# Performance work log

Measured on AMD Instinct MI355X. Metric: run time of the kernel, lower is better.

Reference implementation:

```python
import jax, jax.numpy as jnp
import numpy as np
from jax import lax

EPS = 1e-06
S = 0.025
ALPHA = 0.98
DELTA = 2.0
R = 0.5


def setup_inputs() -> dict:
    key = jax.random.key(0)
    # magnitude spectrogram: [batch, freq, time], nonnegative
    x = jax.random.uniform(key, (32, 256, 4096), dtype=jnp.float32)
    return {"x": x}


def reference(x):
    # x: [B, F, T]; EMA smoother runs over the time axis (last dim).
    # m_0 = s*x_0 ; m_t = (1-s)*m_{t-1} + s*x_t  (init carry 0 reproduces m_0 = s*x_0)
    xt = jnp.moveaxis(x, 2, 0)  # [T, B, F]

    def step(m, frame):
        m = (1.0 - S) * m + S * frame
        return m, m

    _, M = lax.scan(step, jnp.zeros_like(xt[0]), xt)  # [T, B, F]
    M = jnp.moveaxis(M, 0, 2)  # [B, F, T]
    # power-law compression fused elementwise
    return (x / (M + EPS) ** ALPHA + DELTA) ** R - DELTA ** R
```

## Files before the change

### kernel.cpp

```cpp
#include <hip/hip_runtime.h>


constexpr int T_LEN  = 4096;
constexpr int LANES  = 64;
constexpr int QUADS  = 4;
constexpr int PER_LANE = QUADS * 4;
constexpr int CHUNK  = LANES * PER_LANE;
constexpr int CHUNK_F4 = CHUNK / 4;
constexpr int NCHUNK = T_LEN / CHUNK;
constexpr int WAVES_PER_BLK = 4;
constexpr int NTHR   = LANES * WAVES_PER_BLK;

constexpr float EPSF = 1e-6f;
constexpr float SF   = 0.025f;
constexpr float A1F  = 0.975f;

constexpr double dA1    = 0.975;
constexpr double dA2    = dA1 * dA1;
constexpr double dA4    = dA2 * dA2;
constexpr double dA8    = dA4 * dA4;
constexpr double dA16   = dA8 * dA8;
constexpr double dA32   = dA16 * dA16;
constexpr double dA64   = dA32 * dA32;
constexpr double dA128  = dA64 * dA64;
constexpr double dA256  = dA128 * dA128;
constexpr double dA512  = dA256 * dA256;
constexpr double dA1024 = dA512 * dA512;

__global__ __launch_bounds__(NTHR, 6) void pcen_wave_kernel(
    const float* __restrict__ x, float* __restrict__ out, int rows)
{
    const int lane = threadIdx.x & 63;
    const int wave = threadIdx.x >> 6;
    const int row  = blockIdx.x * WAVES_PER_BLK + wave;
    if (row >= rows) return;

    const long long base = (long long)row * T_LEN;
    const float4* __restrict__ px   = (const float4*)(x + base);
    float4* __restrict__       pout = (float4*)(out + base);

    const float cA16  = (float)dA16;
    const float cA32  = (float)dA32;
    const float cA64  = (float)dA64;
    const float cA128 = (float)dA128;
    const float cA256 = (float)dA256;
    const float cA512 = (float)dA512;
    const float cA1024 = (float)dA1024;

    float flane = 1.0f;
    if (lane & 1)  flane *= cA16;
    if (lane & 2)  flane *= cA32;
    if (lane & 4)  flane *= cA64;
    if (lane & 8)  flane *= cA128;
    if (lane & 16) flane *= cA256;
    if (lane & 32) flane *= cA512;

    const float SQRT_D = 1.41421356237309515f;

    float4 buf[QUADS];
    {
        const float4* p = px + lane * QUADS;
#pragma unroll
        for (int j = 0; j < QUADS; ++j) buf[j] = p[j];
    }

    float carry = 0.0f;

#pragma unroll
    for (int c = 0; c < NCHUNK; ++c) {
        float4 nxt[QUADS];
        if (c < NCHUNK - 1) {
            const float4* p = px + (c + 1) * CHUNK_F4 + lane * QUADS;
#pragma unroll
            for (int j = 0; j < QUADS; ++j) nxt[j] = p[j];
        }

        float m = 0.0f;
#pragma unroll
        for (int j = 0; j < QUADS; ++j) {
            m = fmaf(A1F, m, SF * buf[j].x);
            m = fmaf(A1F, m, SF * buf[j].y);
            m = fmaf(A1F, m, SF * buf[j].z);
            m = fmaf(A1F, m, SF * buf[j].w);
        }
        float Sv = m;

        float t;
        t = __shfl_up(Sv, 1,  64); if (lane >= 1)  Sv = fmaf(cA16,  t, Sv);
        t = __shfl_up(Sv, 2,  64); if (lane >= 2)  Sv = fmaf(cA32,  t, Sv);
        t = __shfl_up(Sv, 4,  64); if (lane >= 4)  Sv = fmaf(cA64,  t, Sv);
        t = __shfl_up(Sv, 8,  64); if (lane >= 8)  Sv = fmaf(cA128, t, Sv);
        t = __shfl_up(Sv, 16, 64); if (lane >= 16) Sv = fmaf(cA256, t, Sv);
        t = __shfl_up(Sv, 32, 64); if (lane >= 32) Sv = fmaf(cA512, t, Sv);

        float excl = __shfl_up(Sv, 1, 64);
        if (lane == 0) excl = 0.0f;

        m = fmaf(flane, carry, excl);

        float last = __shfl(Sv, 63, 64);
        carry = fmaf(cA1024, carry, last);

        float4* q = pout + c * CHUNK_F4 + lane * QUADS;
#pragma unroll
        for (int j = 0; j < QUADS; ++j) {
            float4 v = buf[j];
            float4 o;
            m = fmaf(A1F, m, SF * v.x);
            o.x = __builtin_amdgcn_sqrtf(
                      fmaf(v.x, __builtin_amdgcn_exp2f(
                          -0.98f * __builtin_amdgcn_logf(m + EPSF)), 2.0f)) - SQRT_D;
            m = fmaf(A1F, m, SF * v.y);
            o.y = __builtin_amdgcn_sqrtf(
                      fmaf(v.y, __builtin_amdgcn_exp2f(
                          -0.98f * __builtin_amdgcn_logf(m + EPSF)), 2.0f)) - SQRT_D;
            m = fmaf(A1F, m, SF * v.z);
            o.z = __builtin_amdgcn_sqrtf(
                      fmaf(v.z, __builtin_amdgcn_exp2f(
                          -0.98f * __builtin_amdgcn_logf(m + EPSF)), 2.0f)) - SQRT_D;
            m = fmaf(A1F, m, SF * v.w);
            o.w = __builtin_amdgcn_sqrtf(
                      fmaf(v.w, __builtin_amdgcn_exp2f(
                          -0.98f * __builtin_amdgcn_logf(m + EPSF)), 2.0f)) - SQRT_D;
            q[j] = o;
        }

#pragma unroll
        for (int j = 0; j < QUADS; ++j) buf[j] = nxt[j];
    }
}

extern "C" void kernel_launch(void* const* d_in, const int* in_sizes, int n_in,
                              void* d_out, int out_size, void* d_ws, size_t ws_size,
                              hipStream_t stream) {
    const float* x = (const float*)d_in[0];
    float* out = (float*)d_out;
    const int rows = in_sizes[0] / T_LEN;
    const int blocks = (rows + WAVES_PER_BLK - 1) / WAVES_PER_BLK;
    pcen_wave_kernel<<<dim3(blocks), dim3(NTHR), 0, stream>>>(x, out, rows);
}
```

Measured before the change: 244.7 us.

## Use lane-contiguous float4 tiles with four independent wave scans per tile

Changes the per-lane data assignment so each lane owns one float4 per 256-element sub-tile, making each wave load and store fully contiguous 1 KB segments instead of each lane reading 64 contiguous bytes. It runs four independent shuffle scans per tile, which gives more ILP, and rescales the decay powers to match 4 elements per lane. It also raises the launch-bounds occupancy hint from 6 to 8. The cost is four times as many cross-lane shuffles per tile and a serial carry chain across the sub-tiles.

```diff
diff --git a/kernel.cpp b/kernel.cpp
--- a/kernel.cpp
+++ b/kernel.cpp
@@ -1,33 +1,30 @@
 #include <hip/hip_runtime.h>
 
 
-constexpr int T_LEN  = 4096;
-constexpr int LANES  = 64;
-constexpr int QUADS  = 4;
-constexpr int PER_LANE = QUADS * 4;
-constexpr int CHUNK  = LANES * PER_LANE;
-constexpr int CHUNK_F4 = CHUNK / 4;
-constexpr int NCHUNK = T_LEN / CHUNK;
+constexpr int T_LEN   = 4096;
+constexpr int LANES   = 64;
+constexpr int SUBS    = 4;
+constexpr int TILE    = LANES * 4 * SUBS;
+constexpr int TILE_F4 = TILE / 4;
+constexpr int NTILE   = T_LEN / TILE;
 constexpr int WAVES_PER_BLK = 4;
-constexpr int NTHR   = LANES * WAVES_PER_BLK;
+constexpr int NTHR    = LANES * WAVES_PER_BLK;
 
 constexpr float EPSF = 1e-6f;
 constexpr float SF   = 0.025f;
 constexpr float A1F  = 0.975f;
 
-constexpr double dA1    = 0.975;
-constexpr double dA2    = dA1 * dA1;
-constexpr double dA4    = dA2 * dA2;
-constexpr double dA8    = dA4 * dA4;
-constexpr double dA16   = dA8 * dA8;
-constexpr double dA32   = dA16 * dA16;
-constexpr double dA64   = dA32 * dA32;
-constexpr double dA128  = dA64 * dA64;
-constexpr double dA256  = dA128 * dA128;
-constexpr double dA512  = dA256 * dA256;
-constexpr double dA1024 = dA512 * dA512;
+constexpr double dA1   = 0.975;
+constexpr double dA2   = dA1 * dA1;
+constexpr double dA4   = dA2 * dA2;
+constexpr double dA8   = dA4 * dA4;
+constexpr double dA16  = dA8 * dA8;
+constexpr double dA32  = dA16 * dA16;
+constexpr double dA64  = dA32 * dA32;
+constexpr double dA128 = dA64 * dA64;
+constexpr double dA256 = dA128 * dA128;
 
-__global__ __launch_bounds__(NTHR, 6) void pcen_wave_kernel(
+__global__ __launch_bounds__(NTHR, 8) void pcen_wave_kernel(
     const float* __restrict__ x, float* __restrict__ out, int rows)
 {
     const int lane = threadIdx.x & 63;
@@ -39,72 +36,74 @@
     const float4* __restrict__ px   = (const float4*)(x + base);
     float4* __restrict__       pout = (float4*)(out + base);
 
+    const float cA4   = (float)dA4;
+    const float cA8   = (float)dA8;
     const float cA16  = (float)dA16;
     const float cA32  = (float)dA32;
     const float cA64  = (float)dA64;
     const float cA128 = (float)dA128;
     const float cA256 = (float)dA256;
-    const float cA512 = (float)dA512;
-    const float cA1024 = (float)dA1024;
 
     float flane = 1.0f;
-    if (lane & 1)  flane *= cA16;
-    if (lane & 2)  flane *= cA32;
-    if (lane & 4)  flane *= cA64;
-    if (lane & 8)  flane *= cA128;
-    if (lane & 16) flane *= cA256;
-    if (lane & 32) flane *= cA512;
+    if (lane & 1)  flane *= cA4;
+    if (lane & 2)  flane *= cA8;
+    if (lane & 4)  flane *= cA16;
+    if (lane & 8)  flane *= cA32;
+    if (lane & 16) flane *= cA64;
+    if (lane & 32) flane *= cA128;
 
     const float SQRT_D = 1.41421356237309515f;
 
-    float4 buf[QUADS];
-    {
-        const float4* p = px + lane * QUADS;
+    float4 buf[SUBS];
 #pragma unroll
-        for (int j = 0; j < QUADS; ++j) buf[j] = p[j];
-    }
+    for (int j = 0; j < SUBS; ++j) buf[j] = px[j * LANES + lane];
 
     float carry = 0.0f;
 
 #pragma unroll
-    for (int c = 0; c < NCHUNK; ++c) {
-        float4 nxt[QUADS];
-        if (c < NCHUNK - 1) {
-            const float4* p = px + (c + 1) * CHUNK_F4 + lane * QUADS;
+    for (int t = 0; t < NTILE; ++t) {
+        float4 nxt[SUBS];
+        if (t < NTILE - 1) {
 #pragma unroll
-            for (int j = 0; j < QUADS; ++j) nxt[j] = p[j];
+            for (int j = 0; j < SUBS; ++j)
+                nxt[j] = px[(t + 1) * TILE_F4 + j * LANES + lane];
         }
 
-        float m = 0.0f;
+        float Sv[SUBS];
 #pragma unroll
-        for (int j = 0; j < QUADS; ++j) {
-            m = fmaf(A1F, m, SF * buf[j].x);
+        for (int j = 0; j < SUBS; ++j) {
+            float m = SF * buf[j].x;
             m = fmaf(A1F, m, SF * buf[j].y);
             m = fmaf(A1F, m, SF * buf[j].z);
             m = fmaf(A1F, m, SF * buf[j].w);
+            Sv[j] = m;
         }
-        float Sv = m;
 
-        float t;
-        t = __shfl_up(Sv, 1,  64); if (lane >= 1)  Sv = fmaf(cA16,  t, Sv);
-        t = __shfl_up(Sv, 2,  64); if (lane >= 2)  Sv = fmaf(cA32,  t, Sv);
-        t = __shfl_up(Sv, 4,  64); if (lane >= 4)  Sv = fmaf(cA64,  t, Sv);
-        t = __shfl_up(Sv, 8,  64); if (lane >= 8)  Sv = fmaf(cA128, t, Sv);
-        t = __shfl_up(Sv, 16, 64); if (lane >= 16) Sv = fmaf(cA256, t, Sv);
-        t = __shfl_up(Sv, 32, 64); if (lane >= 32) Sv = fmaf(cA512, t, Sv);
+#pragma unroll
+        for (int j = 0; j < SUBS; ++j) {
+            float tt;
+            tt = __shfl_up(Sv[j], 1,  64); if (lane >= 1)  Sv[j] = fmaf(cA4,   tt, Sv[j]);
+            tt = __shfl_up(Sv[j], 2,  64); if (lane >= 2)  Sv[j] = fmaf(cA8,   tt, Sv[j]);
+            tt = __shfl_up(Sv[j], 4,  64); if (lane >= 4)  Sv[j] = fmaf(cA16,  tt, Sv[j]);
+            tt = __shfl_up(Sv[j], 8,  64); if (lane >= 8)  Sv[j] = fmaf(cA32,  tt, Sv[j]);
+            tt = __shfl_up(Sv[j], 16, 64); if (lane >= 16) Sv[j] = fmaf(cA64,  tt, Sv[j]);
+            tt = __shfl_up(Sv[j], 32, 64); if (lane >= 32) Sv[j] = fmaf(cA128, tt, Sv[j]);
+        }
 
-        float excl = __shfl_up(Sv, 1, 64);
-        if (lane == 0) excl = 0.0f;
+        float seed[SUBS];
+#pragma unroll
+        for (int j = 0; j < SUBS; ++j) {
+            float excl = __shfl_up(Sv[j], 1, 64);
+            if (lane == 0) excl = 0.0f;
+            float last = __shfl(Sv[j], 63, 64);
+            seed[j] = fmaf(flane, carry, excl);
+            carry   = fmaf(cA256, carry, last);
+        }
 
-        m = fmaf(flane, carry, excl);
-
-        float last = __shfl(Sv, 63, 64);
-        carry = fmaf(cA1024, carry, last);
-
-        float4* q = pout + c * CHUNK_F4 + lane * QUADS;
 #pragma unroll
-        for (int j = 0; j < QUADS; ++j) {
+        for (int j = 0; j < SUBS; ++j) {
             float4 v = buf[j];
+            float  m = seed[j];
             float4 o;
             m = fmaf(A1F, m, SF * v.x);
             o.x = __builtin_amdgcn_sqrtf(
@@ -122,11 +121,11 @@
             o.w = __builtin_amdgcn_sqrtf(
                       fmaf(v.w, __builtin_amdgcn_exp2f(
                           -0.98f * __builtin_amdgcn_logf(m + EPSF)), 2.0f)) - SQRT_D;
-            q[j] = o;
+            pout[t * TILE_F4 + j * LANES + lane] = o;
         }
 
 #pragma unroll
-        for (int j = 0; j < QUADS; ++j) buf[j] = nxt[j];
+        for (int j = 0; j < SUBS; ++j) buf[j] = nxt[j];
     }
 }
 
```

After: 232.4 us. 1.05x faster.
